# Optimization experiments

Hardware: AMD Instinct MI355X
Metric: run time of the kernel (lower is better)

Reference implementation:

```python
import jax, jax.numpy as jnp
import numpy as np

DIM = 16
HID = 32
DIAG_MIN, DIAG_MAX = 0.316, 3.16


def setup_inputs() -> dict:
    key = jax.random.key(0)
    k0, k1, k2, k3, k4, k5 = jax.random.split(key, 6)
    B, N, M, D = 2, 256, 256, DIM
    x1 = jax.random.normal(k0, (B, N, 1, D), dtype=jnp.float32)
    x2 = jax.random.normal(k1, (B, 1, M, D), dtype=jnp.float32)
    # MLP params: Linear(D, HID) then Linear(HID, D*D), torch layout (out, in)
    W1 = jax.random.normal(k2, (HID, D), dtype=jnp.float32) * 0.1
    b1 = jax.random.normal(k3, (HID,), dtype=jnp.float32) * 0.01
    W2 = jax.random.normal(k4, (D * D, HID), dtype=jnp.float32) * 0.1
    b2 = jax.random.normal(k5, (D * D,), dtype=jnp.float32) * 0.01
    return {"x1": x1, "x2": x2, "W1": W1, "b1": b1, "W2": W2, "b2": b2}


def _cholesky_factor(x, W1, b1, W2, b2):
    # x: (..., D) -> L: (..., D, D)
    D = x.shape[-1]
    dt = x.dtype
    I = jnp.eye(D, dtype=dt)               # diag mask / identity I_bias
    tril = jnp.tril(jnp.ones((D, D), dt))  # lower-tri mask
    h = jax.nn.silu(x @ W1.T + b1)         # (..., HID)
    raw = h @ W2.T + b2                    # (..., D*D)
    L = raw.reshape(*x.shape[:-1], D, D) + I  # I_bias = identity (default)
    L = L * tril
    L = L * (1.0 - I) + jax.nn.softplus(L) * I
    diag = jnp.clip(jnp.diagonal(L, axis1=-2, axis2=-1), DIAG_MIN, DIAG_MAX)
    L = L * (1.0 - I) + diag[..., None] * I  # diag_embed(clamped diag)
    return L


def reference(x1, x2, W1, b1, W2, b2):
    dx = x2 - x1                 # (B, N, M, D) via broadcast
    mid = (x1 + x2) * 0.5        # (B, N, M, D)
    L = _cholesky_factor(mid, W1, b1, W2, b2)      # (B, N, M, D, D)
    G = jnp.einsum('...ik,...jk->...ij', L, L)     # G = L @ L^T, SPD
    dist_sq = jnp.einsum('...i,...ij,...j->...', dx, G, dx)  # Mahalanobis
    return jnp.sqrt(jnp.clip(dist_sq, 1e-6, None))  # (B, N, M)
```

## Files before the change

kernel.cpp:

```cpp
#include <hip/hip_runtime.h>
#include <math.h>

#define DIMD 16
#define HIDN 32
#define DIAG_MIN 0.316f
#define DIAG_MAX 3.16f
#define NT 9
#define PLSTRIDE 68
#define HSTRIDE 36
#define DXSTRIDE 20
#define TRI(i) (((i)*((i)+1))>>1)

typedef short bf16x8 __attribute__((ext_vector_type(8)));
typedef float f32x4  __attribute__((ext_vector_type(4)));

__device__ const unsigned char R_OF_RC[136] = {
    0,
    16,17,
    32,33,34,
    48,49,50,51,
    64,65,66,67,68,
    80,81,82,83,84,85,
    96,97,98,99,100,101,102,
    112,113,114,115,116,117,118,119,
    128,129,130,131,132,133,134,135,136,
    144,145,146,147,148,149,150,151,152,153,
    160,161,162,163,164,165,166,167,168,169,170,
    176,177,178,179,180,181,182,183,184,185,186,187,
    192,193,194,195,196,197,198,199,200,201,202,203,204,
    208,209,210,211,212,213,214,215,216,217,218,219,220,221,
    224,225,226,227,228,229,230,231,232,233,234,235,236,237,238,
    240,241,242,243,244,245,246,247,248,249,250,251,252,253,254,255
};

__device__ __forceinline__ short f2bf(float f) {
    unsigned u = __float_as_uint(f);
    return (short)((u + 0x7FFFu + ((u >> 16) & 1u)) >> 16);
}
__device__ __forceinline__ float bf2f(short s) {
    return __uint_as_float(((unsigned)(unsigned short)s) << 16);
}
__device__ __forceinline__ unsigned pk(float a, float b) {
    return (unsigned)(unsigned short)f2bf(a) | ((unsigned)(unsigned short)f2bf(b) << 16);
}
__device__ __forceinline__ float silu(float x) {
    return x * __frcp_rn(1.0f + __expf(-x));
}

template<int KK>
__device__ __forceinline__ float combine(const short* __restrict__ Pm,
                                         const float* __restrict__ dxr)
{
    float distp = 0.0f;
    #pragma unroll
    for (int qq = 0; qq < 4; ++qq) {
        const int k = KK + 4 * qq;
        float r = bf2f(Pm[(TRI(k) + k) * PLSTRIDE]) + 1.0f;
        float sp = __logf(1.0f + __expf(r));
        float dg = fminf(fmaxf(sp, DIAG_MIN), DIAG_MAX);
        float y = dxr[k] * dg;
        #pragma unroll
        for (int i = k + 1; i < DIMD; ++i)
            y = fmaf(dxr[i], bf2f(Pm[(TRI(i) + k) * PLSTRIDE]), y);
        distp = fmaf(y, y, distp);
    }
    return distp;
}

__global__ __launch_bounds__(256, 4) void rm_kernel(
    const float* __restrict__ x1, const float* __restrict__ x2,
    const float* __restrict__ W1, const float* __restrict__ b1,
    const float* __restrict__ W2, const float* __restrict__ b2,
    float* __restrict__ out)
{
    __shared__ __align__(16) char uni[136 * PLSTRIDE * 2];
    __shared__ short hls[4 * 16 * HSTRIDE];
    __shared__ float dxs[64 * DXSTRIDE];
    __shared__ float part[256];
    short* w2t = (short*)uni;
    float* b2c = (float*)(uni + 9216);
    short* Pl  = (short*)uni;

    const int tid  = threadIdx.x;
    const int lane = tid & 63;
    const int wid  = tid >> 6;
    const int blk  = blockIdx.x;
    const int mc   = blk & 3;
    const int bn   = blk >> 2;
    const int b    = bn >> 8;

    const int arow = lane & 15;
    const int kgrp = lane >> 4;
    const int m_loc = wid * 16 + arow;
    const int m     = mc * 64 + m_loc;

    #pragma unroll
    for (int it = 0; it < 2; ++it) {
        const int rc = it * 128 + (tid >> 1);
        if (rc < 144) {
            const int rcs = rc > 135 ? 135 : rc;
            const int r = R_OF_RC[rcs];
            const int half = tid & 1;
            const float4* s4 = (const float4*)(W2 + r * HIDN + half * 16);
            float4 v0 = s4[0], v1 = s4[1], v2 = s4[2], v3 = s4[3];
            uint4 wa, wb;
            wa.x = pk(v0.x, v0.y); wa.y = pk(v0.z, v0.w);
            wa.z = pk(v1.x, v1.y); wa.w = pk(v1.z, v1.w);
            wb.x = pk(v2.x, v2.y); wb.y = pk(v2.z, v2.w);
            wb.z = pk(v3.x, v3.y); wb.w = pk(v3.z, v3.w);
            const int base = (((rc >> 4) * 4 + half * 2) * 16 + (rc & 15)) * 8;
            *(uint4*)(w2t + base)       = wa;
            *(uint4*)(w2t + base + 128) = wb;
        }
    }
    if (tid < 144) b2c[tid] = b2[R_OF_RC[tid > 135 ? 135 : tid]];

    const float4* a4 = (const float4*)(x1 + bn * DIMD);
    const float4* c4 = (const float4*)(x2 + (b * 256 + m) * DIMD);
    float mid[DIMD];
    #pragma unroll
    for (int q = 0; q < 4; ++q) {
        float4 va = a4[q], vb = c4[q];
        mid[4*q+0] = (va.x + vb.x) * 0.5f;
        mid[4*q+1] = (va.y + vb.y) * 0.5f;
        mid[4*q+2] = (va.z + vb.z) * 0.5f;
        mid[4*q+3] = (va.w + vb.w) * 0.5f;
        if (kgrp == 0) {
            float4 v = {vb.x - va.x, vb.y - va.y, vb.z - va.z, vb.w - va.w};
            *(float4*)(&dxs[m_loc * DXSTRIDE + 4 * q]) = v;
        }
    }

    bf16x8 Bm;
    #pragma unroll
    for (int jo = 0; jo < 8; ++jo) {
        float v = kgrp == 0 ? mid[jo] : (kgrp == 1 ? mid[8 + jo] : 0.0f);
        Bm[jo] = f2bf(v);
    }
    #pragma unroll
    for (int t = 0; t < 2; ++t) {
        bf16x8 Aw = {0, 0, 0, 0, 0, 0, 0, 0};
        if (kgrp < 2) {
            const float4* wp = (const float4*)(W1 + (t * 16 + arow) * DIMD + kgrp * 8);
            float4 a = wp[0], bb = wp[1];
            Aw[0] = f2bf(a.x);  Aw[1] = f2bf(a.y);  Aw[2] = f2bf(a.z);  Aw[3] = f2bf(a.w);
            Aw[4] = f2bf(bb.x); Aw[5] = f2bf(bb.y); Aw[6] = f2bf(bb.z); Aw[7] = f2bf(bb.w);
        }
        float4 cb = *(const float4*)(b1 + t * 16 + kgrp * 4);
        f32x4 c0 = {cb.x, cb.y, cb.z, cb.w};
        f32x4 hr = __builtin_amdgcn_mfma_f32_16x16x32_bf16(Aw, Bm, c0, 0, 0, 0);
        uint2 hw;
        hw.x = pk(silu(hr[0]), silu(hr[1]));
        hw.y = pk(silu(hr[2]), silu(hr[3]));
        *(uint2*)(hls + wid * 16 * HSTRIDE + arow * HSTRIDE + t * 16 + kgrp * 4) = hw;
    }

    bf16x8 A2;
    {
        const uint2* hp = (const uint2*)(hls + wid * 16 * HSTRIDE + arow * HSTRIDE + kgrp * 8);
        uint2 p0 = hp[0], p1 = hp[1];
        uint4 tmp = {p0.x, p0.y, p1.x, p1.y};
        A2 = *(bf16x8*)&tmp;
    }

    __syncthreads();

    f32x4 acc[NT];
    #pragma unroll
    for (int t = 0; t < NT; ++t) {
        bf16x8 B2 = *(const bf16x8*)(w2t + ((t * 4 + kgrp) * 16 + arow) * 8);
        const float cb = b2c[t * 16 + arow];
        f32x4 c0 = {cb, cb, cb, cb};
        acc[t] = __builtin_amdgcn_mfma_f32_16x16x32_bf16(A2, B2, c0, 0, 0, 0);
    }

    __syncthreads();

    #pragma unroll
    for (int t = 0; t < NT; ++t) {
        int rc = t * 16 + arow;
        rc = rc > 135 ? 135 : rc;
        uint2 v;
        v.x = pk(acc[t][0], acc[t][1]);
        v.y = pk(acc[t][2], acc[t][3]);
        *(uint2*)(&Pl[rc * PLSTRIDE + wid * 16 + kgrp * 4]) = v;
    }

    __syncthreads();

    const int cm = tid & 63;
    const int kk = __builtin_amdgcn_readfirstlane(tid >> 6);
    const short* Pm = Pl + cm;

    float dxr[DIMD];
    #pragma unroll
    for (int q = 0; q < 4; ++q) {
        float4 v = *(const float4*)(&dxs[cm * DXSTRIDE + 4 * q]);
        dxr[4*q+0] = v.x; dxr[4*q+1] = v.y; dxr[4*q+2] = v.z; dxr[4*q+3] = v.w;
    }

    float distp;
    switch (kk) {
        case 0:  distp = combine<0>(Pm, dxr); break;
        case 1:  distp = combine<1>(Pm, dxr); break;
        case 2:  distp = combine<2>(Pm, dxr); break;
        default: distp = combine<3>(Pm, dxr); break;
    }
    part[tid] = distp;

    __syncthreads();

    if (tid < 64) {
        float d = part[tid] + part[64 + tid] + part[128 + tid] + part[192 + tid];
        out[bn * 256 + mc * 64 + tid] = __fsqrt_rn(fmaxf(d, 1e-6f));
    }
}

extern "C" void kernel_launch(void* const* d_in, const int* in_sizes, int n_in,
                              void* d_out, int out_size, void* d_ws, size_t ws_size,
                              hipStream_t stream) {
    const float* x1 = (const float*)d_in[0];
    const float* x2 = (const float*)d_in[1];
    const float* W1 = (const float*)d_in[2];
    const float* b1 = (const float*)d_in[3];
    const float* W2 = (const float*)d_in[4];
    const float* b2 = (const float*)d_in[5];
    float* out = (float*)d_out;

    rm_kernel<<<2048, 256, 0, stream>>>(x1, x2, W1, b1, W2, b2, out);
}
```

Baseline: 18.82 us.

## Process two m-chunks per block, reusing W2 fragments held in registers

The grid is halved and each block now loops over two 64-column chunks of m. The bf16 W2 tile and the b2 bias values are staged once, then kept in registers (B2 fragments and b2v) across both chunks instead of being re-read from shared memory. This amortizes the per-block W2 conversion and staging cost and removes one barrier per chunk. In exchange it uses more registers and serializes two chunks inside a block, which lowers block-level parallelism.

```diff
diff --git a/kernel.cpp b/kernel.cpp
--- a/kernel.cpp
+++ b/kernel.cpp
@@ -78,21 +78,18 @@
     __shared__ float dxs[64 * DXSTRIDE];
     __shared__ float part[256];
     short* w2t = (short*)uni;
-    float* b2c = (float*)(uni + 9216);
     short* Pl  = (short*)uni;
 
     const int tid  = threadIdx.x;
     const int lane = tid & 63;
     const int wid  = tid >> 6;
     const int blk  = blockIdx.x;
-    const int mc   = blk & 3;
-    const int bn   = blk >> 2;
+    const int half = blk & 1;
+    const int bn   = blk >> 1;
     const int b    = bn >> 8;
 
     const int arow = lane & 15;
     const int kgrp = lane >> 4;
-    const int m_loc = wid * 16 + arow;
-    const int m     = mc * 64 + m_loc;
 
     #pragma unroll
     for (int it = 0; it < 2; ++it) {
@@ -100,119 +97,140 @@
         if (rc < 144) {
             const int rcs = rc > 135 ? 135 : rc;
             const int r = R_OF_RC[rcs];
-            const int half = tid & 1;
-            const float4* s4 = (const float4*)(W2 + r * HIDN + half * 16);
+            const int hf = tid & 1;
+            const float4* s4 = (const float4*)(W2 + r * HIDN + hf * 16);
             float4 v0 = s4[0], v1 = s4[1], v2 = s4[2], v3 = s4[3];
             uint4 wa, wb;
             wa.x = pk(v0.x, v0.y); wa.y = pk(v0.z, v0.w);
             wa.z = pk(v1.x, v1.y); wa.w = pk(v1.z, v1.w);
             wb.x = pk(v2.x, v2.y); wb.y = pk(v2.z, v2.w);
             wb.z = pk(v3.x, v3.y); wb.w = pk(v3.z, v3.w);
-            const int base = (((rc >> 4) * 4 + half * 2) * 16 + (rc & 15)) * 8;
+            const int base = (((rc >> 4) * 4 + hf * 2) * 16 + (rc & 15)) * 8;
             *(uint4*)(w2t + base)       = wa;
             *(uint4*)(w2t + base + 128) = wb;
         }
     }
-    if (tid < 144) b2c[tid] = b2[R_OF_RC[tid > 135 ? 135 : tid]];
 
     const float4* a4 = (const float4*)(x1 + bn * DIMD);
-    const float4* c4 = (const float4*)(x2 + (b * 256 + m) * DIMD);
-    float mid[DIMD];
-    #pragma unroll
-    for (int q = 0; q < 4; ++q) {
-        float4 va = a4[q], vb = c4[q];
-        mid[4*q+0] = (va.x + vb.x) * 0.5f;
-        mid[4*q+1] = (va.y + vb.y) * 0.5f;
-        mid[4*q+2] = (va.z + vb.z) * 0.5f;
-        mid[4*q+3] = (va.w + vb.w) * 0.5f;
-        if (kgrp == 0) {
-            float4 v = {vb.x - va.x, vb.y - va.y, vb.z - va.z, vb.w - va.w};
-            *(float4*)(&dxs[m_loc * DXSTRIDE + 4 * q]) = v;
-        }
-    }
-
-    bf16x8 Bm;
-    #pragma unroll
-    for (int jo = 0; jo < 8; ++jo) {
-        float v = kgrp == 0 ? mid[jo] : (kgrp == 1 ? mid[8 + jo] : 0.0f);
-        Bm[jo] = f2bf(v);
-    }
-    #pragma unroll
-    for (int t = 0; t < 2; ++t) {
-        bf16x8 Aw = {0, 0, 0, 0, 0, 0, 0, 0};
-        if (kgrp < 2) {
-            const float4* wp = (const float4*)(W1 + (t * 16 + arow) * DIMD + kgrp * 8);
-            float4 a = wp[0], bb = wp[1];
-            Aw[0] = f2bf(a.x);  Aw[1] = f2bf(a.y);  Aw[2] = f2bf(a.z);  Aw[3] = f2bf(a.w);
-            Aw[4] = f2bf(bb.x); Aw[5] = f2bf(bb.y); Aw[6] = f2bf(bb.z); Aw[7] = f2bf(bb.w);
-        }
-        float4 cb = *(const float4*)(b1 + t * 16 + kgrp * 4);
-        f32x4 c0 = {cb.x, cb.y, cb.z, cb.w};
-        f32x4 hr = __builtin_amdgcn_mfma_f32_16x16x32_bf16(Aw, Bm, c0, 0, 0, 0);
-        uint2 hw;
-        hw.x = pk(silu(hr[0]), silu(hr[1]));
-        hw.y = pk(silu(hr[2]), silu(hr[3]));
-        *(uint2*)(hls + wid * 16 * HSTRIDE + arow * HSTRIDE + t * 16 + kgrp * 4) = hw;
-    }
-
-    bf16x8 A2;
-    {
-        const uint2* hp = (const uint2*)(hls + wid * 16 * HSTRIDE + arow * HSTRIDE + kgrp * 8);
-        uint2 p0 = hp[0], p1 = hp[1];
-        uint4 tmp = {p0.x, p0.y, p1.x, p1.y};
-        A2 = *(bf16x8*)&tmp;
-    }
-
-    __syncthreads();
-
-    f32x4 acc[NT];
-    #pragma unroll
-    for (int t = 0; t < NT; ++t) {
-        bf16x8 B2 = *(const bf16x8*)(w2t + ((t * 4 + kgrp) * 16 + arow) * 8);
-        const float cb = b2c[t * 16 + arow];
-        f32x4 c0 = {cb, cb, cb, cb};
-        acc[t] = __builtin_amdgcn_mfma_f32_16x16x32_bf16(A2, B2, c0, 0, 0, 0);
-    }
-
-    __syncthreads();
-
+    float4 va0 = a4[0], va1 = a4[1], va2 = a4[2], va3 = a4[3];
+
+    float b2v[NT];
     #pragma unroll
     for (int t = 0; t < NT; ++t) {
         int rc = t * 16 + arow;
-        rc = rc > 135 ? 135 : rc;
-        uint2 v;
-        v.x = pk(acc[t][0], acc[t][1]);
-        v.y = pk(acc[t][2], acc[t][3]);
-        *(uint2*)(&Pl[rc * PLSTRIDE + wid * 16 + kgrp * 4]) = v;
+        b2v[t] = b2[R_OF_RC[rc > 135 ? 135 : rc]];
     }
 
     __syncthreads();
 
-    const int cm = tid & 63;
-    const int kk = __builtin_amdgcn_readfirstlane(tid >> 6);
-    const short* Pm = Pl + cm;
-
-    float dxr[DIMD];
-    #pragma unroll
-    for (int q = 0; q < 4; ++q) {
-        float4 v = *(const float4*)(&dxs[cm * DXSTRIDE + 4 * q]);
-        dxr[4*q+0] = v.x; dxr[4*q+1] = v.y; dxr[4*q+2] = v.z; dxr[4*q+3] = v.w;
-    }
-
-    float distp;
-    switch (kk) {
-        case 0:  distp = combine<0>(Pm, dxr); break;
-        case 1:  distp = combine<1>(Pm, dxr); break;
-        case 2:  distp = combine<2>(Pm, dxr); break;
-        default: distp = combine<3>(Pm, dxr); break;
-    }
-    part[tid] = distp;
+    bf16x8 B2[NT];
+    #pragma unroll
+    for (int t = 0; t < NT; ++t)
+        B2[t] = *(const bf16x8*)(w2t + ((t * 4 + kgrp) * 16 + arow) * 8);
 
     __syncthreads();
 
-    if (tid < 64) {
-        float d = part[tid] + part[64 + tid] + part[128 + tid] + part[192 + tid];
-        out[bn * 256 + mc * 64 + tid] = __fsqrt_rn(fmaxf(d, 1e-6f));
+    #pragma unroll 1
+    for (int c = 0; c < 2; ++c) {
+        const int m_loc = wid * 16 + arow;
+        const int m     = half * 128 + c * 64 + m_loc;
+
+        const float4* c4 = (const float4*)(x2 + (b * 256 + m) * DIMD);
+        float mid[DIMD];
+        {
+            float4 vb0 = c4[0], vb1 = c4[1], vb2 = c4[2], vb3 = c4[3];
+            mid[0]  = (va0.x + vb0.x) * 0.5f;  mid[1]  = (va0.y + vb0.y) * 0.5f;
+            mid[2]  = (va0.z + vb0.z) * 0.5f;  mid[3]  = (va0.w + vb0.w) * 0.5f;
+            mid[4]  = (va1.x + vb1.x) * 0.5f;  mid[5]  = (va1.y + vb1.y) * 0.5f;
+            mid[6]  = (va1.z + vb1.z) * 0.5f;  mid[7]  = (va1.w + vb1.w) * 0.5f;
+            mid[8]  = (va2.x + vb2.x) * 0.5f;  mid[9]  = (va2.y + vb2.y) * 0.5f;
+            mid[10] = (va2.z + vb2.z) * 0.5f;  mid[11] = (va2.w + vb2.w) * 0.5f;
+            mid[12] = (va3.x + vb3.x) * 0.5f;  mid[13] = (va3.y + vb3.y) * 0.5f;
+            mid[14] = (va3.z + vb3.z) * 0.5f;  mid[15] = (va3.w + vb3.w) * 0.5f;
+            if (kgrp == 0) {
+                float4 d0 = {vb0.x - va0.x, vb0.y - va0.y, vb0.z - va0.z, vb0.w - va0.w};
+                float4 d1 = {vb1.x - va1.x, vb1.y - va1.y, vb1.z - va1.z, vb1.w - va1.w};
+                float4 d2 = {vb2.x - va2.x, vb2.y - va2.y, vb2.z - va2.z, vb2.w - va2.w};
+                float4 d3 = {vb3.x - va3.x, vb3.y - va3.y, vb3.z - va3.z, vb3.w - va3.w};
+                *(float4*)(&dxs[m_loc * DXSTRIDE +  0]) = d0;
+                *(float4*)(&dxs[m_loc * DXSTRIDE +  4]) = d1;
+                *(float4*)(&dxs[m_loc * DXSTRIDE +  8]) = d2;
+                *(float4*)(&dxs[m_loc * DXSTRIDE + 12]) = d3;
+            }
+        }
+
+        bf16x8 Bm;
+        #pragma unroll
+        for (int jo = 0; jo < 8; ++jo) {
+            float v = kgrp == 0 ? mid[jo] : (kgrp == 1 ? mid[8 + jo] : 0.0f);
+            Bm[jo] = f2bf(v);
+        }
+        #pragma unroll
+        for (int t = 0; t < 2; ++t) {
+            bf16x8 Aw = {0, 0, 0, 0, 0, 0, 0, 0};
+            if (kgrp < 2) {
+                const float4* wp = (const float4*)(W1 + (t * 16 + arow) * DIMD + kgrp * 8);
+                float4 a = wp[0], bb = wp[1];
+                Aw[0] = f2bf(a.x);  Aw[1] = f2bf(a.y);  Aw[2] = f2bf(a.z);  Aw[3] = f2bf(a.w);
+                Aw[4] = f2bf(bb.x); Aw[5] = f2bf(bb.y); Aw[6] = f2bf(bb.z); Aw[7] = f2bf(bb.w);
+            }
+            float4 cb = *(const float4*)(b1 + t * 16 + kgrp * 4);
+            f32x4 c0 = {cb.x, cb.y, cb.z, cb.w};
+            f32x4 hr = __builtin_amdgcn_mfma_f32_16x16x32_bf16(Aw, Bm, c0, 0, 0, 0);
+            uint2 hw;
+            hw.x = pk(silu(hr[0]), silu(hr[1]));
+            hw.y = pk(silu(hr[2]), silu(hr[3]));
+            *(uint2*)(hls + wid * 16 * HSTRIDE + arow * HSTRIDE + t * 16 + kgrp * 4) = hw;
+        }
+
+        bf16x8 A2;
+        {
+            const uint2* hp = (const uint2*)(hls + wid * 16 * HSTRIDE + arow * HSTRIDE + kgrp * 8);
+            uint2 p0 = hp[0], p1 = hp[1];
+            uint4 tmp = {p0.x, p0.y, p1.x, p1.y};
+            A2 = *(bf16x8*)&tmp;
+        }
+
+        #pragma unroll
+        for (int t = 0; t < NT; ++t) {
+            f32x4 c0 = {b2v[t], b2v[t], b2v[t], b2v[t]};
+            f32x4 acc = __builtin_amdgcn_mfma_f32_16x16x32_bf16(A2, B2[t], c0, 0, 0, 0);
+            int rc = t * 16 + arow;
+            rc = rc > 135 ? 135 : rc;
+            uint2 v;
+            v.x = pk(acc[0], acc[1]);
+            v.y = pk(acc[2], acc[3]);
+            *(uint2*)(&Pl[rc * PLSTRIDE + wid * 16 + kgrp * 4]) = v;
+        }
+
+        __syncthreads();
+
+        const int cm = lane;
+        const int kk = __builtin_amdgcn_readfirstlane(wid);
+        const short* Pm = Pl + cm;
+
+        float dxr[DIMD];
+        #pragma unroll
+        for (int q = 0; q < 4; ++q) {
+            float4 v = *(const float4*)(&dxs[cm * DXSTRIDE + 4 * q]);
+            dxr[4*q+0] = v.x; dxr[4*q+1] = v.y; dxr[4*q+2] = v.z; dxr[4*q+3] = v.w;
+        }
+
+        float distp;
+        switch (kk) {
+            case 0:  distp = combine<0>(Pm, dxr); break;
+            case 1:  distp = combine<1>(Pm, dxr); break;
+            case 2:  distp = combine<2>(Pm, dxr); break;
+            default: distp = combine<3>(Pm, dxr); break;
+        }
+        part[tid] = distp;
+
+        __syncthreads();
+
+        if (tid < 64) {
+            float d = part[tid] + part[64 + tid] + part[128 + tid] + part[192 + tid];
+            out[bn * 256 + half * 128 + c * 64 + tid] = __fsqrt_rn(fmaxf(d, 1e-6f));
+        }
     }
 }
 
@@ -227,5 +245,5 @@
     const float* b2 = (const float*)d_in[5];
     float* out = (float*)d_out;
 
-    rm_kernel<<<2048, 256, 0, stream>>>(x1, x2, W1, b1, W2, b2, out);
-}
+    rm_kernel<<<1024, 256, 0, stream>>>(x1, x2, W1, b1, W2, b2, out);
+}
```

Result: slower. 20.80 us (+10.5%).

## Shuffle hidden activations via bpermute, store dx as bf16, raise occupancy

Applied to the files above, without the earlier changes.

The kernel drops the LDS staging buffer for hidden activations and rebuilds the second MFMA's A operand with ds_bpermute lane shuffles. The dx vector is now stored in LDS as bf16 rather than fp32. The b2 bias is held in per-thread registers instead of LDS. The second GEMM now writes results straight to Pl, which removes one barrier, but w2t and Pl become separate LDS buffers instead of an aliased union. Launch bounds rise to five blocks per CU, trading register pressure and extra dx quantization error for occupancy and fewer barriers.

```diff
diff --git a/kernel.cpp b/kernel.cpp
--- a/kernel.cpp
+++ b/kernel.cpp
@@ -7,7 +7,6 @@
 #define DIAG_MAX 3.16f
 #define NT 9
 #define PLSTRIDE 68
-#define HSTRIDE 36
 #define DXSTRIDE 20
 #define TRI(i) (((i)*((i)+1))>>1)
 
@@ -37,8 +36,8 @@
     unsigned u = __float_as_uint(f);
     return (short)((u + 0x7FFFu + ((u >> 16) & 1u)) >> 16);
 }
-__device__ __forceinline__ float bf2f(short s) {
-    return __uint_as_float(((unsigned)(unsigned short)s) << 16);
+__device__ __forceinline__ float bf2f(unsigned short s) {
+    return __uint_as_float(((unsigned)s) << 16);
 }
 __device__ __forceinline__ unsigned pk(float a, float b) {
     return (unsigned)(unsigned short)f2bf(a) | ((unsigned)(unsigned short)f2bf(b) << 16);
@@ -55,31 +54,28 @@
     #pragma unroll
     for (int qq = 0; qq < 4; ++qq) {
         const int k = KK + 4 * qq;
-        float r = bf2f(Pm[(TRI(k) + k) * PLSTRIDE]) + 1.0f;
+        float r = bf2f((unsigned short)Pm[(TRI(k) + k) * PLSTRIDE]) + 1.0f;
         float sp = __logf(1.0f + __expf(r));
         float dg = fminf(fmaxf(sp, DIAG_MIN), DIAG_MAX);
         float y = dxr[k] * dg;
         #pragma unroll
         for (int i = k + 1; i < DIMD; ++i)
-            y = fmaf(dxr[i], bf2f(Pm[(TRI(i) + k) * PLSTRIDE]), y);
+            y = fmaf(dxr[i], bf2f((unsigned short)Pm[(TRI(i) + k) * PLSTRIDE]), y);
         distp = fmaf(y, y, distp);
     }
     return distp;
 }
 
-__global__ __launch_bounds__(256, 4) void rm_kernel(
+__global__ __launch_bounds__(256, 5) void rm_kernel(
     const float* __restrict__ x1, const float* __restrict__ x2,
     const float* __restrict__ W1, const float* __restrict__ b1,
     const float* __restrict__ W2, const float* __restrict__ b2,
     float* __restrict__ out)
 {
-    __shared__ __align__(16) char uni[136 * PLSTRIDE * 2];
-    __shared__ short hls[4 * 16 * HSTRIDE];
-    __shared__ float dxs[64 * DXSTRIDE];
+    __shared__ __align__(16) short w2t[4608];
+    __shared__ __align__(16) short Pl[136 * PLSTRIDE];
+    __shared__ __align__(16) short dxs[64 * DXSTRIDE];
     __shared__ float part[256];
-    short* w2t = (short*)uni;
-    float* b2c = (float*)(uni + 9216);
-    short* Pl  = (short*)uni;
 
     const int tid  = threadIdx.x;
     const int lane = tid & 63;
@@ -89,8 +85,8 @@
     const int bn   = blk >> 2;
     const int b    = bn >> 8;
 
-    const int arow = lane & 15;
-    const int kgrp = lane >> 4;
+    const int arow  = lane & 15;
+    const int kgrp  = lane >> 4;
     const int m_loc = wid * 16 + arow;
     const int m     = mc * 64 + m_loc;
 
@@ -100,35 +96,46 @@
         if (rc < 144) {
             const int rcs = rc > 135 ? 135 : rc;
             const int r = R_OF_RC[rcs];
-            const int half = tid & 1;
-            const float4* s4 = (const float4*)(W2 + r * HIDN + half * 16);
+            const int hf = tid & 1;
+            const float4* s4 = (const float4*)(W2 + r * HIDN + hf * 16);
             float4 v0 = s4[0], v1 = s4[1], v2 = s4[2], v3 = s4[3];
             uint4 wa, wb;
             wa.x = pk(v0.x, v0.y); wa.y = pk(v0.z, v0.w);
             wa.z = pk(v1.x, v1.y); wa.w = pk(v1.z, v1.w);
             wb.x = pk(v2.x, v2.y); wb.y = pk(v2.z, v2.w);
             wb.z = pk(v3.x, v3.y); wb.w = pk(v3.z, v3.w);
-            const int base = (((rc >> 4) * 4 + half * 2) * 16 + (rc & 15)) * 8;
+            const int base = (((rc >> 4) * 4 + hf * 2) * 16 + (rc & 15)) * 8;
             *(uint4*)(w2t + base)       = wa;
             *(uint4*)(w2t + base + 128) = wb;
         }
     }
-    if (tid < 144) b2c[tid] = b2[R_OF_RC[tid > 135 ? 135 : tid]];
+
+    float b2v[NT];
+    #pragma unroll
+    for (int t = 0; t < NT; ++t) {
+        int rc = t * 16 + arow;
+        b2v[t] = b2[R_OF_RC[rc > 135 ? 135 : rc]];
+    }
 
     const float4* a4 = (const float4*)(x1 + bn * DIMD);
     const float4* c4 = (const float4*)(x2 + (b * 256 + m) * DIMD);
-    float mid[DIMD];
+    float mid[DIMD], dxv[DIMD];
     #pragma unroll
     for (int q = 0; q < 4; ++q) {
         float4 va = a4[q], vb = c4[q];
-        mid[4*q+0] = (va.x + vb.x) * 0.5f;
-        mid[4*q+1] = (va.y + vb.y) * 0.5f;
-        mid[4*q+2] = (va.z + vb.z) * 0.5f;
-        mid[4*q+3] = (va.w + vb.w) * 0.5f;
-        if (kgrp == 0) {
-            float4 v = {vb.x - va.x, vb.y - va.y, vb.z - va.z, vb.w - va.w};
-            *(float4*)(&dxs[m_loc * DXSTRIDE + 4 * q]) = v;
-        }
+        mid[4*q+0] = (va.x + vb.x) * 0.5f;  dxv[4*q+0] = vb.x - va.x;
+        mid[4*q+1] = (va.y + vb.y) * 0.5f;  dxv[4*q+1] = vb.y - va.y;
+        mid[4*q+2] = (va.z + vb.z) * 0.5f;  dxv[4*q+2] = vb.z - va.z;
+        mid[4*q+3] = (va.w + vb.w) * 0.5f;  dxv[4*q+3] = vb.w - va.w;
+    }
+    if (kgrp == 0) {
+        uint4 da, db;
+        da.x = pk(dxv[0],  dxv[1]);  da.y = pk(dxv[2],  dxv[3]);
+        da.z = pk(dxv[4],  dxv[5]);  da.w = pk(dxv[6],  dxv[7]);
+        db.x = pk(dxv[8],  dxv[9]);  db.y = pk(dxv[10], dxv[11]);
+        db.z = pk(dxv[12], dxv[13]); db.w = pk(dxv[14], dxv[15]);
+        *(uint4*)(&dxs[m_loc * DXSTRIDE])     = da;
+        *(uint4*)(&dxs[m_loc * DXSTRIDE + 8]) = db;
     }
 
     bf16x8 Bm;
@@ -137,6 +144,7 @@
         float v = kgrp == 0 ? mid[jo] : (kgrp == 1 ? mid[8 + jo] : 0.0f);
         Bm[jo] = f2bf(v);
     }
+    uint2 p0, p1;
     #pragma unroll
     for (int t = 0; t < 2; ++t) {
         bf16x8 Aw = {0, 0, 0, 0, 0, 0, 0, 0};
@@ -152,51 +160,63 @@
         uint2 hw;
         hw.x = pk(silu(hr[0]), silu(hr[1]));
         hw.y = pk(silu(hr[2]), silu(hr[3]));
-        *(uint2*)(hls + wid * 16 * HSTRIDE + arow * HSTRIDE + t * 16 + kgrp * 4) = hw;
+        if (t == 0) p0 = hw; else p1 = hw;
     }
 
     bf16x8 A2;
     {
-        const uint2* hp = (const uint2*)(hls + wid * 16 * HSTRIDE + arow * HSTRIDE + kgrp * 8);
-        uint2 p0 = hp[0], p1 = hp[1];
-        uint4 tmp = {p0.x, p0.y, p1.x, p1.y};
+        const int ad0 = (((kgrp & 1) << 5) + arow) << 2;
+        const int ad1 = ad0 + 64;
+        int w0a = __builtin_amdgcn_ds_bpermute(ad0, (int)p0.x);
+        int w0b = __builtin_amdgcn_ds_bpermute(ad0, (int)p1.x);
+        int w1a = __builtin_amdgcn_ds_bpermute(ad0, (int)p0.y);
+        int w1b = __builtin_amdgcn_ds_bpermute(ad0, (int)p1.y);
+        int w2a = __builtin_amdgcn_ds_bpermute(ad1, (int)p0.x);
+        int w2b = __builtin_amdgcn_ds_bpermute(ad1, (int)p1.x);
+        int w3a = __builtin_amdgcn_ds_bpermute(ad1, (int)p0.y);
+        int w3b = __builtin_amdgcn_ds_bpermute(ad1, (int)p1.y);
+        const bool lo = kgrp < 2;
+        uint4 tmp;
+        tmp.x = lo ? (unsigned)w0a : (unsigned)w0b;
+        tmp.y = lo ? (unsigned)w1a : (unsigned)w1b;
+        tmp.z = lo ? (unsigned)w2a : (unsigned)w2b;
+        tmp.w = lo ? (unsigned)w3a : (unsigned)w3b;
         A2 = *(bf16x8*)&tmp;
     }
 
     __syncthreads();
 
-    f32x4 acc[NT];
     #pragma unroll
     for (int t = 0; t < NT; ++t) {
         bf16x8 B2 = *(const bf16x8*)(w2t + ((t * 4 + kgrp) * 16 + arow) * 8);
-        const float cb = b2c[t * 16 + arow];
-        f32x4 c0 = {cb, cb, cb, cb};
-        acc[t] = __builtin_amdgcn_mfma_f32_16x16x32_bf16(A2, B2, c0, 0, 0, 0);
-    }
-
-    __syncthreads();
-
-    #pragma unroll
-    for (int t = 0; t < NT; ++t) {
+        f32x4 c0 = {b2v[t], b2v[t], b2v[t], b2v[t]};
+        f32x4 acc = __builtin_amdgcn_mfma_f32_16x16x32_bf16(A2, B2, c0, 0, 0, 0);
         int rc = t * 16 + arow;
         rc = rc > 135 ? 135 : rc;
         uint2 v;
-        v.x = pk(acc[t][0], acc[t][1]);
-        v.y = pk(acc[t][2], acc[t][3]);
+        v.x = pk(acc[0], acc[1]);
+        v.y = pk(acc[2], acc[3]);
         *(uint2*)(&Pl[rc * PLSTRIDE + wid * 16 + kgrp * 4]) = v;
     }
 
     __syncthreads();
 
-    const int cm = tid & 63;
-    const int kk = __builtin_amdgcn_readfirstlane(tid >> 6);
+    const int cm = lane;
+    const int kk = __builtin_amdgcn_readfirstlane(wid);
     const short* Pm = Pl + cm;
 
     float dxr[DIMD];
-    #pragma unroll
-    for (int q = 0; q < 4; ++q) {
-        float4 v = *(const float4*)(&dxs[cm * DXSTRIDE + 4 * q]);
-        dxr[4*q+0] = v.x; dxr[4*q+1] = v.y; dxr[4*q+2] = v.z; dxr[4*q+3] = v.w;
+    {
+        uint4 da = *(const uint4*)(&dxs[cm * DXSTRIDE]);
+        uint4 db = *(const uint4*)(&dxs[cm * DXSTRIDE + 8]);
+        dxr[0]  = bf2f((unsigned short)(da.x & 0xFFFF)); dxr[1]  = bf2f((unsigned short)(da.x >> 16));
+        dxr[2]  = bf2f((unsigned short)(da.y & 0xFFFF)); dxr[3]  = bf2f((unsigned short)(da.y >> 16));
+        dxr[4]  = bf2f((unsigned short)(da.z & 0xFFFF)); dxr[5]  = bf2f((unsigned short)(da.z >> 16));
+        dxr[6]  = bf2f((unsigned short)(da.w & 0xFFFF)); dxr[7]  = bf2f((unsigned short)(da.w >> 16));
+        dxr[8]  = bf2f((unsigned short)(db.x & 0xFFFF)); dxr[9]  = bf2f((unsigned short)(db.x >> 16));
+        dxr[10] = bf2f((unsigned short)(db.y & 0xFFFF)); dxr[11] = bf2f((unsigned short)(db.y >> 16));
+        dxr[12] = bf2f((unsigned short)(db.z & 0xFFFF)); dxr[13] = bf2f((unsigned short)(db.z >> 16));
+        dxr[14] = bf2f((unsigned short)(db.w & 0xFFFF)); dxr[15] = bf2f((unsigned short)(db.w >> 16));
     }
 
     float distp;
```

Result: slower. 20.12 us (+6.9%).

## Fuse L^T·dx contraction into MFMA epilogue using selector-matrix MFMAs

Applied to the files above, without the earlier changes.

Computes the second MLP layer with the lower-triangular weights as the A operand, so each lane holds accumulator entries for its own m. The softplus/clamp diagonal and the dx scaling are applied in registers, and a constant 0/1 selector matrix in LDS sums the terms per column k with another MFMA. This removes the bf16 P staging in LDS, the hidden-activation LDS round trip, the scalar combine loop and two of the block barriers. The cost is extra MFMAs, bf16 rounding of the products, and a selector table built by every block. Occupancy target is raised to 5 blocks per CU.

```diff
diff --git a/kernel.cpp b/kernel.cpp
--- a/kernel.cpp
+++ b/kernel.cpp
@@ -1,15 +1,8 @@
 #include <hip/hip_runtime.h>
 #include <math.h>
 
-#define DIMD 16
-#define HIDN 32
 #define DIAG_MIN 0.316f
 #define DIAG_MAX 3.16f
-#define NT 9
-#define PLSTRIDE 68
-#define HSTRIDE 36
-#define DXSTRIDE 20
-#define TRI(i) (((i)*((i)+1))>>1)
 
 typedef short bf16x8 __attribute__((ext_vector_type(8)));
 typedef float f32x4  __attribute__((ext_vector_type(4)));
@@ -32,14 +25,52 @@
     224,225,226,227,228,229,230,231,232,233,234,235,236,237,238,
     240,241,242,243,244,245,246,247,248,249,250,251,252,253,254,255
 };
+__device__ const unsigned char K_OF_RC[136] = {
+    0,
+    0,1,
+    0,1,2,
+    0,1,2,3,
+    0,1,2,3,4,
+    0,1,2,3,4,5,
+    0,1,2,3,4,5,6,
+    0,1,2,3,4,5,6,7,
+    0,1,2,3,4,5,6,7,8,
+    0,1,2,3,4,5,6,7,8,9,
+    0,1,2,3,4,5,6,7,8,9,10,
+    0,1,2,3,4,5,6,7,8,9,10,11,
+    0,1,2,3,4,5,6,7,8,9,10,11,12,
+    0,1,2,3,4,5,6,7,8,9,10,11,12,13,
+    0,1,2,3,4,5,6,7,8,9,10,11,12,13,14,
+    0,1,2,3,4,5,6,7,8,9,10,11,12,13,14,15
+};
+constexpr unsigned char I_C[144] = {
+    0,
+    1,1,
+    2,2,2,
+    3,3,3,3,
+    4,4,4,4,4,
+    5,5,5,5,5,5,
+    6,6,6,6,6,6,6,
+    7,7,7,7,7,7,7,7,
+    8,8,8,8,8,8,8,8,8,
+    9,9,9,9,9,9,9,9,9,9,
+    10,10,10,10,10,10,10,10,10,10,10,
+    11,11,11,11,11,11,11,11,11,11,11,11,
+    12,12,12,12,12,12,12,12,12,12,12,12,12,
+    13,13,13,13,13,13,13,13,13,13,13,13,13,13,
+    14,14,14,14,14,14,14,14,14,14,14,14,14,14,14,
+    15,15,15,15,15,15,15,15,15,15,15,15,15,15,15,15,
+    0,0,0,0,0,0,0,0
+};
+constexpr unsigned char DM_C[9][4] = {
+    {1,6,9,0},{2,0,0,4},{8,0,0,1},{0,0,2,0},{0,9,0,0},
+    {0,0,4,0},{4,0,0,0},{0,0,0,2},{0,0,0,2}
+};
 
 __device__ __forceinline__ short f2bf(float f) {
     unsigned u = __float_as_uint(f);
     return (short)((u + 0x7FFFu + ((u >> 16) & 1u)) >> 16);
 }
-__device__ __forceinline__ float bf2f(short s) {
-    return __uint_as_float(((unsigned)(unsigned short)s) << 16);
-}
 __device__ __forceinline__ unsigned pk(float a, float b) {
     return (unsigned)(unsigned short)f2bf(a) | ((unsigned)(unsigned short)f2bf(b) << 16);
 }
@@ -47,39 +78,41 @@
     return x * __frcp_rn(1.0f + __expf(-x));
 }
 
-template<int KK>
-__device__ __forceinline__ float combine(const short* __restrict__ Pm,
-                                         const float* __restrict__ dxr)
-{
-    float distp = 0.0f;
-    #pragma unroll
-    for (int qq = 0; qq < 4; ++qq) {
-        const int k = KK + 4 * qq;
-        float r = bf2f(Pm[(TRI(k) + k) * PLSTRIDE]) + 1.0f;
-        float sp = __logf(1.0f + __expf(r));
-        float dg = fminf(fmaxf(sp, DIAG_MIN), DIAG_MAX);
-        float y = dxr[k] * dg;
-        #pragma unroll
-        for (int i = k + 1; i < DIMD; ++i)
-            y = fmaf(dxr[i], bf2f(Pm[(TRI(i) + k) * PLSTRIDE]), y);
-        distp = fmaf(y, y, distp);
-    }
-    return distp;
-}
-
-__global__ __launch_bounds__(256, 4) void rm_kernel(
+template<int T>
+__device__ __forceinline__ uint2 epi(f32x4 acc, int kgrp, const float (&dxv)[16]) {
+    float z[4];
+#define EPIQ(Q)                                                              \
+    {                                                                        \
+        float p = acc[Q];                                                    \
+        constexpr int dm = DM_C[T][Q];                                       \
+        if constexpr (dm != 0) {                                             \
+            float sp = __logf(1.0f + __expf(p + 1.0f));                      \
+            sp = fminf(fmaxf(sp, DIAG_MIN), DIAG_MAX);                       \
+            p = ((dm >> kgrp) & 1) ? sp : p;                                 \
+        }                                                                    \
+        constexpr int i0 = I_C[16*T + Q],     i1 = I_C[16*T + 4 + Q];        \
+        constexpr int i2 = I_C[16*T + 8 + Q], i3 = I_C[16*T + 12 + Q];       \
+        float ds = kgrp == 0 ? dxv[i0]                                       \
+                 : (kgrp == 1 ? dxv[i1] : (kgrp == 2 ? dxv[i2] : dxv[i3]));  \
+        z[Q] = p * ds;                                                       \
+    }
+    EPIQ(0) EPIQ(1) EPIQ(2) EPIQ(3)
+#undef EPIQ
+    uint2 w;
+    w.x = pk(z[0], z[1]);
+    w.y = pk(z[2], z[3]);
+    return w;
+}
+
+__global__ __launch_bounds__(256, 5) void rm_kernel(
     const float* __restrict__ x1, const float* __restrict__ x2,
     const float* __restrict__ W1, const float* __restrict__ b1,
     const float* __restrict__ W2, const float* __restrict__ b2,
     float* __restrict__ out)
 {
-    __shared__ __align__(16) char uni[136 * PLSTRIDE * 2];
-    __shared__ short hls[4 * 16 * HSTRIDE];
-    __shared__ float dxs[64 * DXSTRIDE];
-    __shared__ float part[256];
-    short* w2t = (short*)uni;
-    float* b2c = (float*)(uni + 9216);
-    short* Pl  = (short*)uni;
+    __shared__ __align__(16) short w2t[4608];
+    __shared__ __align__(16) float b2c[144];
+    __shared__ uint4 Elds[320];
 
     const int tid  = threadIdx.x;
     const int lane = tid & 63;
@@ -91,8 +124,7 @@
 
     const int arow = lane & 15;
     const int kgrp = lane >> 4;
-    const int m_loc = wid * 16 + arow;
-    const int m     = mc * 64 + m_loc;
+    const int m    = mc * 64 + wid * 16 + arow;
 
     #pragma unroll
     for (int it = 0; it < 2; ++it) {
@@ -100,35 +132,46 @@
         if (rc < 144) {
             const int rcs = rc > 135 ? 135 : rc;
             const int r = R_OF_RC[rcs];
-            const int half = tid & 1;
-            const float4* s4 = (const float4*)(W2 + r * HIDN + half * 16);
+            const int hf = tid & 1;
+            const float4* s4 = (const float4*)(W2 + r * 32 + hf * 16);
             float4 v0 = s4[0], v1 = s4[1], v2 = s4[2], v3 = s4[3];
-            uint4 wa, wb;
-            wa.x = pk(v0.x, v0.y); wa.y = pk(v0.z, v0.w);
-            wa.z = pk(v1.x, v1.y); wa.w = pk(v1.z, v1.w);
-            wb.x = pk(v2.x, v2.y); wb.y = pk(v2.z, v2.w);
-            wb.z = pk(v3.x, v3.y); wb.w = pk(v3.z, v3.w);
-            const int base = (((rc >> 4) * 4 + half * 2) * 16 + (rc & 15)) * 8;
-            *(uint4*)(w2t + base)       = wa;
-            *(uint4*)(w2t + base + 128) = wb;
+            short* base = w2t + (((rc >> 4) * 4) * 16 + (rc & 15)) * 8 + 4 * hf;
+            uint2 w0 = {pk(v0.x, v0.y), pk(v0.z, v0.w)};
+            uint2 w1 = {pk(v1.x, v1.y), pk(v1.z, v1.w)};
+            uint2 w2v = {pk(v2.x, v2.y), pk(v2.z, v2.w)};
+            uint2 w3 = {pk(v3.x, v3.y), pk(v3.z, v3.w)};
+            *(uint2*)(base)             = w0;
+            *(uint2*)(base + 16 * 8)    = w1;
+            *(uint2*)(base + 32 * 8)    = w2v;
+            *(uint2*)(base + 48 * 8)    = w3;
         }
     }
     if (tid < 144) b2c[tid] = b2[R_OF_RC[tid > 135 ? 135 : tid]];
 
-    const float4* a4 = (const float4*)(x1 + bn * DIMD);
-    const float4* c4 = (const float4*)(x2 + (b * 256 + m) * DIMD);
-    float mid[DIMD];
+    for (int p = tid; p < 320; p += 256) {
+        const int c = p >> 6, ls = p & 63, ar = ls & 15, kg = ls >> 4;
+        unsigned wv[4] = {0u, 0u, 0u, 0u};
+        #pragma unroll
+        for (int jo = 0; jo < 8; ++jo) {
+            const int rcp = 32 * c + 16 * (jo >> 2) + 4 * kg + (jo & 3);
+            const unsigned char kk = K_OF_RC[rcp < 136 ? rcp : 135];
+            const unsigned hv = (rcp < 136 && kk == ar) ? 0x3F80u : 0u;
+            wv[jo >> 1] |= hv << (16 * (jo & 1));
+        }
+        uint4 ev = {wv[0], wv[1], wv[2], wv[3]};
+        Elds[p] = ev;
+    }
+
+    const float4* a4 = (const float4*)(x1 + bn * 16);
+    const float4* c4 = (const float4*)(x2 + (b * 256 + m) * 16);
+    float mid[16], dxv[16];
     #pragma unroll
     for (int q = 0; q < 4; ++q) {
         float4 va = a4[q], vb = c4[q];
-        mid[4*q+0] = (va.x + vb.x) * 0.5f;
-        mid[4*q+1] = (va.y + vb.y) * 0.5f;
-        mid[4*q+2] = (va.z + vb.z) * 0.5f;
-        mid[4*q+3] = (va.w + vb.w) * 0.5f;
-        if (kgrp == 0) {
-            float4 v = {vb.x - va.x, vb.y - va.y, vb.z - va.z, vb.w - va.w};
-            *(float4*)(&dxs[m_loc * DXSTRIDE + 4 * q]) = v;
-        }
+        mid[4*q+0] = (va.x + vb.x) * 0.5f;  dxv[4*q+0] = vb.x - va.x;
+        mid[4*q+1] = (va.y + vb.y) * 0.5f;  dxv[4*q+1] = vb.y - va.y;
+        mid[4*q+2] = (va.z + vb.z) * 0.5f;  dxv[4*q+2] = vb.z - va.z;
+        mid[4*q+3] = (va.w + vb.w) * 0.5f;  dxv[4*q+3] = vb.w - va.w;
     }
 
     bf16x8 Bm;
@@ -137,83 +180,62 @@
         float v = kgrp == 0 ? mid[jo] : (kgrp == 1 ? mid[8 + jo] : 0.0f);
         Bm[jo] = f2bf(v);
     }
-    #pragma unroll
-    for (int t = 0; t < 2; ++t) {
+    uint4 hB;
+    #pragma unroll
+    for (int t1 = 0; t1 < 2; ++t1) {
         bf16x8 Aw = {0, 0, 0, 0, 0, 0, 0, 0};
         if (kgrp < 2) {
-            const float4* wp = (const float4*)(W1 + (t * 16 + arow) * DIMD + kgrp * 8);
-            float4 a = wp[0], bb = wp[1];
-            Aw[0] = f2bf(a.x);  Aw[1] = f2bf(a.y);  Aw[2] = f2bf(a.z);  Aw[3] = f2bf(a.w);
-            Aw[4] = f2bf(bb.x); Aw[5] = f2bf(bb.y); Aw[6] = f2bf(bb.z); Aw[7] = f2bf(bb.w);
+            const float4* wp = (const float4*)(W1 + (t1 * 16 + arow) * 16 + kgrp * 8);
+            float4 a = wp[0], bb2 = wp[1];
+            Aw[0] = f2bf(a.x);   Aw[1] = f2bf(a.y);   Aw[2] = f2bf(a.z);   Aw[3] = f2bf(a.w);
+            Aw[4] = f2bf(bb2.x); Aw[5] = f2bf(bb2.y); Aw[6] = f2bf(bb2.z); Aw[7] = f2bf(bb2.w);
         }
-        float4 cb = *(const float4*)(b1 + t * 16 + kgrp * 4);
+        float4 cb = *(const float4*)(b1 + t1 * 16 + kgrp * 4);
         f32x4 c0 = {cb.x, cb.y, cb.z, cb.w};
         f32x4 hr = __builtin_amdgcn_mfma_f32_16x16x32_bf16(Aw, Bm, c0, 0, 0, 0);
-        uint2 hw;
-        hw.x = pk(silu(hr[0]), silu(hr[1]));
-        hw.y = pk(silu(hr[2]), silu(hr[3]));
-        *(uint2*)(hls + wid * 16 * HSTRIDE + arow * HSTRIDE + t * 16 + kgrp * 4) = hw;
-    }
-
-    bf16x8 A2;
-    {
-        const uint2* hp = (const uint2*)(hls + wid * 16 * HSTRIDE + arow * HSTRIDE + kgrp * 8);
-        uint2 p0 = hp[0], p1 = hp[1];
-        uint4 tmp = {p0.x, p0.y, p1.x, p1.y};
-        A2 = *(bf16x8*)&tmp;
-    }
+        unsigned w0 = pk(silu(hr[0]), silu(hr[1]));
+        unsigned w1 = pk(silu(hr[2]), silu(hr[3]));
+        if (t1 == 0) { hB.x = w0; hB.y = w1; } else { hB.z = w0; hB.w = w1; }
+    }
+    const bf16x8 B8h = *(bf16x8*)&hB;
 
     __syncthreads();
 
-    f32x4 acc[NT];
-    #pragma unroll
-    for (int t = 0; t < NT; ++t) {
-        bf16x8 B2 = *(const bf16x8*)(w2t + ((t * 4 + kgrp) * 16 + arow) * 8);
-        const float cb = b2c[t * 16 + arow];
-        f32x4 c0 = {cb, cb, cb, cb};
-        acc[t] = __builtin_amdgcn_mfma_f32_16x16x32_bf16(A2, B2, c0, 0, 0, 0);
-    }
-
-    __syncthreads();
-
-    #pragma unroll
-    for (int t = 0; t < NT; ++t) {
-        int rc = t * 16 + arow;
-        rc = rc > 135 ? 135 : rc;
-        uint2 v;
-        v.x = pk(acc[t][0], acc[t][1]);
-        v.y = pk(acc[t][2], acc[t][3]);
-        *(uint2*)(&Pl[rc * PLSTRIDE + wid * 16 + kgrp * 4]) = v;
-    }
-
-    __syncthreads();
-
-    const int cm = tid & 63;
-    const int kk = __builtin_amdgcn_readfirstlane(tid >> 6);
-    const short* Pm = Pl + cm;
-
-    float dxr[DIMD];
-    #pragma unroll
-    for (int q = 0; q < 4; ++q) {
-        float4 v = *(const float4*)(&dxs[cm * DXSTRIDE + 4 * q]);
-        dxr[4*q+0] = v.x; dxr[4*q+1] = v.y; dxr[4*q+2] = v.z; dxr[4*q+3] = v.w;
-    }
-
-    float distp;
-    switch (kk) {
-        case 0:  distp = combine<0>(Pm, dxr); break;
-        case 1:  distp = combine<1>(Pm, dxr); break;
-        case 2:  distp = combine<2>(Pm, dxr); break;
-        default: distp = combine<3>(Pm, dxr); break;
-    }
-    part[tid] = distp;
-
-    __syncthreads();
-
-    if (tid < 64) {
-        float d = part[tid] + part[64 + tid] + part[128 + tid] + part[192 + tid];
-        out[bn * 256 + mc * 64 + tid] = __fsqrt_rn(fmaxf(d, 1e-6f));
-    }
+    f32x4 Yacc = {0.0f, 0.0f, 0.0f, 0.0f};
+#define CHUNK(C)                                                              \
+    {                                                                         \
+        uint2 zw0, zw1;                                                       \
+        {                                                                     \
+            bf16x8 a2 = *(const bf16x8*)(w2t + (((2*(C)) * 4 + kgrp) * 16 + arow) * 8); \
+            float4 cb = *(const float4*)(b2c + (2*(C)) * 16 + kgrp * 4);      \
+            f32x4 c0 = {cb.x, cb.y, cb.z, cb.w};                              \
+            f32x4 acc = __builtin_amdgcn_mfma_f32_16x16x32_bf16(a2, B8h, c0, 0, 0, 0); \
+            zw0 = epi<2*(C)>(acc, kgrp, dxv);                                 \
+        }                                                                     \
+        if (2*(C) + 1 < 9) {                                                  \
+            bf16x8 a2 = *(const bf16x8*)(w2t + (((2*(C)+1) * 4 + kgrp) * 16 + arow) * 8); \
+            float4 cb = *(const float4*)(b2c + (2*(C)+1) * 16 + kgrp * 4);    \
+            f32x4 c0 = {cb.x, cb.y, cb.z, cb.w};                              \
+            f32x4 acc = __builtin_amdgcn_mfma_f32_16x16x32_bf16(a2, B8h, c0, 0, 0, 0); \
+            zw1 = epi<(2*(C)+1 < 9 ? 2*(C)+1 : 8)>(acc, kgrp, dxv);           \
+        } else { zw1.x = 0u; zw1.y = 0u; }                                    \
+        uint4 bb = {zw0.x, zw0.y, zw1.x, zw1.y};                              \
+        uint4 ee = Elds[(C) * 64 + lane];                                     \
+        Yacc = __builtin_amdgcn_mfma_f32_16x16x32_bf16(                       \
+            *(bf16x8*)&ee, *(bf16x8*)&bb, Yacc, 0, 0, 0);                     \
+    }
+    CHUNK(0) CHUNK(1) CHUNK(2) CHUNK(3) CHUNK(4)
+#undef CHUNK
+
+    float part = Yacc[0] * Yacc[0];
+    part = fmaf(Yacc[1], Yacc[1], part);
+    part = fmaf(Yacc[2], Yacc[2], part);
+    part = fmaf(Yacc[3], Yacc[3], part);
+    part += __shfl_xor(part, 16, 64);
+    part += __shfl_xor(part, 32, 64);
+
+    if (kgrp == 0)
+        out[bn * 256 + mc * 64 + wid * 16 + arow] = __fsqrt_rn(fmaxf(part, 1e-6f));
 }
 
 extern "C" void kernel_launch(void* const* d_in, const int* in_sizes, int n_in,
```

New measurement: 24.49 us. 30.1% more time.
